# Kernel optimization log

Hardware: AMD Instinct MI355X
Metric: run time of the kernel (lower is better)

## Reference

```python
import jax, jax.numpy as jnp
import numpy as np

B, S, H, NH = 2, 2048, 1024, 16
DK = H // NH


def setup_inputs() -> dict:
    key = jax.random.key(0)
    ks = jax.random.split(key, 11)
    sc = 1.0 / np.sqrt(H)
    return {
        "q": jax.random.normal(ks[0], (B, S, H), jnp.float32),
        "v": jax.random.normal(ks[1], (B, S, H), jnp.float32),
        "k": jax.random.normal(ks[2], (B, S, H), jnp.float32),
        "Wq": jax.random.normal(ks[3], (H, H), jnp.float32) * sc,
        "bq": jax.random.normal(ks[4], (H,), jnp.float32) * 0.01,
        "Wk": jax.random.normal(ks[5], (H, H), jnp.float32) * sc,
        "bk": jax.random.normal(ks[6], (H,), jnp.float32) * 0.01,
        "Wv": jax.random.normal(ks[7], (H, H), jnp.float32) * sc,
        "bv": jax.random.normal(ks[8], (H,), jnp.float32) * 0.01,
        "Wo": jax.random.normal(ks[9], (H, H), jnp.float32) * sc,
        "bo": jax.random.normal(ks[10], (H,), jnp.float32) * 0.01,
    }


def reference(q, v, k, Wq, bq, Wk, bk, Wv, bv, Wo, bo):
    b, s, h = q.shape
    # projections; torch Linear computes x @ W.T + b
    qh = (q @ Wq.T + bq).reshape(b, s, NH, DK).transpose(0, 2, 1, 3)  # [B,NH,S,DK]
    kh = (k @ Wk.T + bk).reshape(b, s, NH, DK).transpose(0, 2, 1, 3)
    vh = (v @ Wv.T + bv).reshape(b, s, NH, DK).transpose(0, 2, 1, 3)
    scores = jnp.einsum("bhqd,bhkd->bhqk", qh, kh) / jnp.sqrt(
        jnp.asarray(DK, qh.dtype))  # [B,NH,S,S]
    probs = jax.nn.softmax(scores, axis=-1)
    ctx = jnp.einsum("bhqk,bhkd->bhqd", probs, vh)  # [B,NH,S,DK]
    concat = ctx.transpose(0, 2, 1, 3).reshape(b, s, h)
    return concat @ Wo.T + bo
```

## Files before the change

### kernel.cpp

```cpp
#include <hip/hip_runtime.h>
#include <cstddef>
#include <cstdint>

typedef _Float16 f16x8 __attribute__((ext_vector_type(8)));
typedef _Float16 f16x4 __attribute__((ext_vector_type(4)));
typedef __fp16   h16x2 __attribute__((ext_vector_type(2)));
typedef float    f32x4 __attribute__((ext_vector_type(4)));

constexpr int B_  = 2;
constexpr int S_  = 2048;
constexpr int H_  = 1024;
constexpr int NH_ = 16;
constexpr int DK_ = 64;
constexpr int M_  = B_ * S_;
constexpr int K_  = H_;

constexpr float SOFF = 4.0f;

#define MFMA32(a, b, c) __builtin_amdgcn_mfma_f32_16x16x32_f16((a), (b), (c), 0, 0, 0)
#define MFMA16(a, b, c) __builtin_amdgcn_mfma_f32_16x16x16f16((a), (b), (c), 0, 0, 0)

__device__ __forceinline__ void glds16(const void* g, void* l) {
    __builtin_amdgcn_global_load_lds(
        (const __attribute__((address_space(1))) void*)g,
        (__attribute__((address_space(3))) void*)l, 16, 0, 0);
}

__device__ __forceinline__ void pk2(f16x4& dst, int half, float a, float b) {
    const h16x2 r = __builtin_amdgcn_cvt_pkrtz(a, b);
    reinterpret_cast<h16x2*>(&dst)[half] = r;
}

struct CvtArgs {
    const float* s[7];
    _Float16*    d[7];
    int          n[7];
};

__global__ __launch_bounds__(256) void cvt7(CvtArgs a)
{
    const int seg = blockIdx.y;
    const int i = (blockIdx.x * 256 + threadIdx.x) * 8;
    if (i + 8 <= a.n[seg]) {
        const float4 v0 = *reinterpret_cast<const float4*>(a.s[seg] + i);
        const float4 v1 = *reinterpret_cast<const float4*>(a.s[seg] + i + 4);
        f16x8 o;
        o[0] = (_Float16)v0.x; o[1] = (_Float16)v0.y;
        o[2] = (_Float16)v0.z; o[3] = (_Float16)v0.w;
        o[4] = (_Float16)v1.x; o[5] = (_Float16)v1.y;
        o[6] = (_Float16)v1.z; o[7] = (_Float16)v1.w;
        *reinterpret_cast<f16x8*>(a.d[seg] + i) = o;
    }
}

struct QkvArgs {
    const _Float16* A[3];
    const _Float16* W[3];
    const float*    bias[3];
    _Float16* dstQ;
    _Float16* dstK;
    _Float16* dstV;
    float qscale;
};

__global__ __launch_bounds__(256) void gemm_qkv(QkvArgs args)
{
    constexpr int BM = 128, BN = 128, BK = 32;
    __shared__ __align__(16) _Float16 sm[8192];
    auto As = reinterpret_cast<_Float16(*)[BK]>(sm);
    auto Ws = reinterpret_cast<_Float16(*)[BK]>(sm + 4096);
    auto Tr = reinterpret_cast<_Float16(*)[64]>(sm);

    const int z = blockIdx.z;
    const _Float16* __restrict__ A = args.A[z];
    const _Float16* __restrict__ W = args.W[z];
    const float* __restrict__ bias = args.bias[z];

    const int t = threadIdx.x;
    const int w = t >> 6, lane = t & 63, quad = lane >> 4, l16 = lane & 15;
    const int m0 = blockIdx.y * BM;
    const int n0 = blockIdx.x * BN;
    const int wr = (w & 1) * 64, wc = (w >> 1) * 64;
    const int srow = lane >> 2, scol = (lane & 3) * 8;

    f32x4 acc[4][4];
#pragma unroll
    for (int i = 0; i < 4; ++i)
#pragma unroll
        for (int j = 0; j < 4; ++j) acc[i][j] = (f32x4){0.f, 0.f, 0.f, 0.f};

    for (int k0 = 0; k0 < K_; k0 += BK) {
        glds16(&A[(size_t)(m0 + w * 32 + srow) * K_ + k0 + scol], &As[w * 32][0]);
        glds16(&A[(size_t)(m0 + w * 32 + 16 + srow) * K_ + k0 + scol], &As[w * 32 + 16][0]);
        glds16(&W[(size_t)(n0 + w * 32 + srow) * K_ + k0 + scol], &Ws[w * 32][0]);
        glds16(&W[(size_t)(n0 + w * 32 + 16 + srow) * K_ + k0 + scol], &Ws[w * 32 + 16][0]);
        __syncthreads();

        f16x8 af[4], bf[4];
#pragma unroll
        for (int i = 0; i < 4; ++i)
            af[i] = *reinterpret_cast<const f16x8*>(&As[wr + i * 16 + l16][quad * 8]);
#pragma unroll
        for (int j = 0; j < 4; ++j)
            bf[j] = *reinterpret_cast<const f16x8*>(&Ws[wc + j * 16 + l16][quad * 8]);
#pragma unroll
        for (int i = 0; i < 4; ++i)
#pragma unroll
            for (int j = 0; j < 4; ++j)
                acc[i][j] = MFMA32(af[i], bf[j], acc[i][j]);
        __syncthreads();
    }

    const float scale = (z == 0) ? args.qscale : 1.0f;
    float bv[4];
#pragma unroll
    for (int j = 0; j < 4; ++j) bv[j] = bias[n0 + wc + j * 16 + l16];

    if (z == 2) {
#pragma unroll
        for (int i = 0; i < 4; ++i) {
            const int sb = m0 + wr + i * 16 + quad * 4;
            const int b = sb >> 11, s = sb & (S_ - 1);
#pragma unroll
            for (int j = 0; j < 4; ++j) {
                const int d = wc + j * 16 + l16;
                const int h = blockIdx.x * 2 + (d >> 6);
                const int dd = d & 63;
                const int kt = s >> 4, dt = dd >> 4;
                f16x4 ov;
#pragma unroll
                for (int r = 0; r < 4; ++r) ov[r] = (_Float16)(acc[i][j][r] + bv[j]);
                _Float16* base = args.dstV +
                    ((((size_t)b * NH_ + h) * 128 + kt) * 4 + dt) * 256;
                *reinterpret_cast<f16x4*>(&base[lane * 4]) = ov;
            }
        }
        return;
    }

    _Float16* dst = (z == 0) ? args.dstQ : args.dstK;
    const int b = m0 >> 11, s0 = m0 & (S_ - 1);
#pragma unroll
    for (int ch = 0; ch < 2; ++ch) {
        __syncthreads();
        if ((w >> 1) == ch) {
#pragma unroll
            for (int i = 0; i < 4; ++i)
#pragma unroll
                for (int j = 0; j < 4; ++j)
#pragma unroll
                    for (int r = 0; r < 4; ++r)
                        Tr[wr + i * 16 + quad * 4 + r][j * 16 + l16] =
                            (_Float16)((acc[i][j][r] + bv[j]) * scale);
        }
        __syncthreads();
        const int h = blockIdx.x * 2 + ch;
        _Float16* dbase = dst + ((size_t)(b * NH_ + h) * S_ + s0) * DK_;
#pragma unroll
        for (int p = 0; p < 4; ++p) {
            const int c = t + p * 256;
            *reinterpret_cast<f16x8*>(&dbase[c * 8]) =
                *reinterpret_cast<const f16x8*>(&Tr[c >> 3][(c & 7) * 8]);
        }
    }
}

__global__ __launch_bounds__(256) void gemm_out(
    const _Float16* __restrict__ A, const _Float16* __restrict__ W,
    const float* __restrict__ bias, float* __restrict__ out)
{
    constexpr int BM = 128, BN = 128, BK = 32;
    __shared__ _Float16 As[BM][BK];
    __shared__ _Float16 Ws[BN][BK];

    const int t = threadIdx.x;
    const int w = t >> 6, lane = t & 63, quad = lane >> 4, l16 = lane & 15;
    const int m0 = blockIdx.y * BM;
    const int n0 = blockIdx.x * BN;
    const int wr = (w & 1) * 64, wc = (w >> 1) * 64;
    const int srow = lane >> 2, scol = (lane & 3) * 8;

    f32x4 acc[4][4];
#pragma unroll
    for (int i = 0; i < 4; ++i)
#pragma unroll
        for (int j = 0; j < 4; ++j) acc[i][j] = (f32x4){0.f, 0.f, 0.f, 0.f};

    for (int k0 = 0; k0 < K_; k0 += BK) {
        glds16(&A[(size_t)(m0 + w * 32 + srow) * K_ + k0 + scol], &As[w * 32][0]);
        glds16(&A[(size_t)(m0 + w * 32 + 16 + srow) * K_ + k0 + scol], &As[w * 32 + 16][0]);
        glds16(&W[(size_t)(n0 + w * 32 + srow) * K_ + k0 + scol], &Ws[w * 32][0]);
        glds16(&W[(size_t)(n0 + w * 32 + 16 + srow) * K_ + k0 + scol], &Ws[w * 32 + 16][0]);
        __syncthreads();

        f16x8 af[4], bf[4];
#pragma unroll
        for (int i = 0; i < 4; ++i)
            af[i] = *reinterpret_cast<const f16x8*>(&As[wr + i * 16 + l16][quad * 8]);
#pragma unroll
        for (int j = 0; j < 4; ++j)
            bf[j] = *reinterpret_cast<const f16x8*>(&Ws[wc + j * 16 + l16][quad * 8]);
#pragma unroll
        for (int i = 0; i < 4; ++i)
#pragma unroll
            for (int j = 0; j < 4; ++j)
                acc[i][j] = MFMA32(af[i], bf[j], acc[i][j]);
        __syncthreads();
    }

    float bv[4];
#pragma unroll
    for (int j = 0; j < 4; ++j) bv[j] = bias[n0 + wc + j * 16 + l16];

#pragma unroll
    for (int i = 0; i < 4; ++i)
#pragma unroll
        for (int j = 0; j < 4; ++j)
#pragma unroll
            for (int r = 0; r < 4; ++r)
                out[(size_t)(m0 + wr + i * 16 + quad * 4 + r) * H_ +
                    n0 + wc + j * 16 + l16] = acc[i][j][r] + bv[j];
}

__global__ __launch_bounds__(256) void attn_mfma(
    const _Float16* __restrict__ qh, const _Float16* __restrict__ kh,
    const _Float16* __restrict__ vfrag, _Float16* __restrict__ ctx)
{
    __shared__ float Ob[4][64][36];
    __shared__ float Ls[4][64];
    __shared__ float Linv[64];

    const int t = threadIdx.x;
    const int w = t >> 6, lane = t & 63, quad = lane >> 4, l16 = lane & 15;
    const int q0 = blockIdx.x * 64;
    const int bh = blockIdx.y;

    const _Float16* qb = qh + (size_t)bh * S_ * DK_;
    const _Float16* kb = kh + (size_t)bh * S_ * DK_;
    const _Float16* vb = vfrag + (size_t)bh * 128 * 4 * 256;

    f16x8 qf[4][2];
#pragma unroll
    for (int qt = 0; qt < 4; ++qt)
#pragma unroll
        for (int h2 = 0; h2 < 2; ++h2)
            qf[qt][h2] = *reinterpret_cast<const f16x8*>(
                &qb[(size_t)(q0 + qt * 16 + l16) * DK_ + h2 * 32 + quad * 8]);

    f32x4 o[4][4];
#pragma unroll
    for (int dt = 0; dt < 4; ++dt)
#pragma unroll
        for (int qt = 0; qt < 4; ++qt) o[dt][qt] = (f32x4){0.f, 0.f, 0.f, 0.f};
    float lp_[4];
#pragma unroll
    for (int qt = 0; qt < 4; ++qt) lp_[qt] = 0.f;

    const _Float16* kptr = kb + (size_t)(w * 16 + l16) * DK_ + quad * 8;
    const _Float16* vptr = vb + (size_t)w * 4 * 256 + lane * 4;

    f16x8 kf0 = *reinterpret_cast<const f16x8*>(kptr);
    f16x8 kf1 = *reinterpret_cast<const f16x8*>(kptr + 32);

    for (int ti = 0; ti < 32; ++ti) {
        f16x4 vf[4];
#pragma unroll
        for (int dt = 0; dt < 4; ++dt)
            vf[dt] = *reinterpret_cast<const f16x4*>(vptr + dt * 256);
        vptr += 4 * 4 * 256;

        const _Float16* nkp = (ti < 31) ? kptr + 64 * DK_ : kptr;
        const f16x8 nk0 = *reinterpret_cast<const f16x8*>(nkp);
        const f16x8 nk1 = *reinterpret_cast<const f16x8*>(nkp + 32);
        kptr = nkp;

        f32x4 sc[4];
#pragma unroll
        for (int qt = 0; qt < 4; ++qt) {
            sc[qt] = (f32x4){-SOFF, -SOFF, -SOFF, -SOFF};
            sc[qt] = MFMA32(kf0, qf[qt][0], sc[qt]);
            sc[qt] = MFMA32(kf1, qf[qt][1], sc[qt]);
        }

        f16x4 pf[4];
#pragma unroll
        for (int qt = 0; qt < 4; ++qt) {
            const float p0 = __builtin_amdgcn_exp2f(sc[qt][0]);
            const float p1 = __builtin_amdgcn_exp2f(sc[qt][1]);
            const float p2 = __builtin_amdgcn_exp2f(sc[qt][2]);
            const float p3 = __builtin_amdgcn_exp2f(sc[qt][3]);
            lp_[qt] += (p0 + p1) + (p2 + p3);
            f16x4 pv;
            pk2(pv, 0, p0, p1);
            pk2(pv, 1, p2, p3);
            pf[qt] = pv;
        }

#pragma unroll
        for (int dt = 0; dt < 4; ++dt)
#pragma unroll
            for (int qt = 0; qt < 4; ++qt)
                o[dt][qt] = MFMA16(vf[dt], pf[qt], o[dt][qt]);

        kf0 = nk0;
        kf1 = nk1;
    }

#pragma unroll
    for (int qt = 0; qt < 4; ++qt) {
        float l = lp_[qt];
        l += __shfl_xor(l, 16);
        l += __shfl_xor(l, 32);
        if (quad == 0) Ls[w][qt * 16 + l16] = l;
    }
    __syncthreads();
    if (t < 64)
        Linv[t] = 1.f / (((Ls[0][t] + Ls[1][t]) + (Ls[2][t] + Ls[3][t])));

    const int b = bh >> 4, hh = bh & 15;
    const int dg = t & 3, qq = t >> 2;
#pragma unroll
    for (int ph = 0; ph < 2; ++ph) {
        __syncthreads();
#pragma unroll
        for (int dl = 0; dl < 2; ++dl) {
            const int dt = ph * 2 + dl;
#pragma unroll
            for (int qt = 0; qt < 4; ++qt)
                *reinterpret_cast<f32x4*>(
                    &Ob[w][qt * 16 + l16][dl * 16 + quad * 4]) = o[dt][qt];
        }
        __syncthreads();
        f32x4 s0 = (f32x4){0.f, 0.f, 0.f, 0.f};
        f32x4 s1 = (f32x4){0.f, 0.f, 0.f, 0.f};
#pragma unroll
        for (int ww = 0; ww < 4; ++ww) {
            s0 += *reinterpret_cast<const f32x4*>(&Ob[ww][qq][dg * 8]);
            s1 += *reinterpret_cast<const f32x4*>(&Ob[ww][qq][dg * 8 + 4]);
        }
        const float li = Linv[qq];
        f16x8 ov;
#pragma unroll
        for (int r = 0; r < 4; ++r) {
            ov[r]     = (_Float16)(s0[r] * li);
            ov[4 + r] = (_Float16)(s1[r] * li);
        }
        *reinterpret_cast<f16x8*>(
            &ctx[((size_t)b * S_ + q0 + qq) * H_ + hh * 64 + ph * 32 + dg * 8]) = ov;
    }
}

extern "C" void kernel_launch(void* const* d_in, const int* in_sizes, int n_in,
                              void* d_out, int out_size, void* d_ws,
                              size_t ws_size, hipStream_t stream)
{
    (void)in_sizes; (void)n_in; (void)out_size; (void)ws_size;
    const float* q  = (const float*)d_in[0];
    const float* v  = (const float*)d_in[1];
    const float* k  = (const float*)d_in[2];
    const float* Wq = (const float*)d_in[3];
    const float* bq = (const float*)d_in[4];
    const float* Wk = (const float*)d_in[5];
    const float* bk = (const float*)d_in[6];
    const float* Wv = (const float*)d_in[7];
    const float* bv = (const float*)d_in[8];
    const float* Wo = (const float*)d_in[9];
    const float* bo = (const float*)d_in[10];
    float* out = (float*)d_out;

    constexpr size_t NACT = (size_t)M_ * K_;
    constexpr size_t NW   = (size_t)H_ * H_;
    _Float16* p = (_Float16*)d_ws;
    _Float16* q16  = p;
    _Float16* k16  = p + NACT;
    _Float16* v16  = p + 2 * NACT;
    _Float16* w16q = p + 3 * NACT;
    _Float16* w16k = w16q + NW;
    _Float16* w16v = w16k + NW;
    _Float16* w16o = w16v + NW;
    _Float16* qhd  = w16o + NW;
    _Float16* khd  = qhd + NACT;
    _Float16* vfr  = khd + NACT;
    _Float16* ctx  = q16;

    CvtArgs ca;
    ca.s[0] = q;  ca.d[0] = q16;  ca.n[0] = (int)NACT;
    ca.s[1] = v;  ca.d[1] = v16;  ca.n[1] = (int)NACT;
    ca.s[2] = k;  ca.d[2] = k16;  ca.n[2] = (int)NACT;
    ca.s[3] = Wq; ca.d[3] = w16q; ca.n[3] = (int)NW;
    ca.s[4] = Wk; ca.d[4] = w16k; ca.n[4] = (int)NW;
    ca.s[5] = Wv; ca.d[5] = w16v; ca.n[5] = (int)NW;
    ca.s[6] = Wo; ca.d[6] = w16o; ca.n[6] = (int)NW;
    cvt7<<<dim3(2048, 7), 256, 0, stream>>>(ca);

    QkvArgs ga;
    ga.A[0] = q16;  ga.W[0] = w16q; ga.bias[0] = bq;
    ga.A[1] = k16;  ga.W[1] = w16k; ga.bias[1] = bk;
    ga.A[2] = v16;  ga.W[2] = w16v; ga.bias[2] = bv;
    ga.dstQ = qhd;  ga.dstK = khd;  ga.dstV = vfr;
    ga.qscale = 0.125f * 1.4426950408889634f;

    gemm_qkv<<<dim3(H_ / 128, M_ / 128, 3), 256, 0, stream>>>(ga);

    attn_mfma<<<dim3(S_ / 64, B_ * NH_), 256, 0, stream>>>(qhd, khd, vfr, ctx);

    gemm_out<<<dim3(H_ / 128, M_ / 128), 256, 0, stream>>>(ctx, w16o, bo, out);
}
```

Baseline: 236.6 us.

## Pipeline QK scores one step ahead, use 32-wide PV MFMA, remap grids

The attention loop now handles two 64-key tiles per iteration. It computes the next pair's QK scores after the PV MFMAs, wrapped in s_setprio, so score MFMAs overlap exp work across iterations. V is stored in a new fragment layout that allows 16x16x32 MFMAs for P·V instead of 16x16x16. The attention grid is flattened and remapped so blocks of the same head land on the same XCD for L2 reuse. The output GEMM tile shrinks to 64x128, doubling block count to improve occupancy at the cost of less reuse per block.

```diff
diff --git a/kernel.cpp b/kernel.cpp
--- a/kernel.cpp
+++ b/kernel.cpp
@@ -6,6 +6,7 @@
 typedef _Float16 f16x4 __attribute__((ext_vector_type(4)));
 typedef __fp16   h16x2 __attribute__((ext_vector_type(2)));
 typedef float    f32x4 __attribute__((ext_vector_type(4)));
+typedef float    f32x2 __attribute__((ext_vector_type(2)));
 
 constexpr int B_  = 2;
 constexpr int S_  = 2048;
@@ -18,17 +19,11 @@
 constexpr float SOFF = 4.0f;
 
 #define MFMA32(a, b, c) __builtin_amdgcn_mfma_f32_16x16x32_f16((a), (b), (c), 0, 0, 0)
-#define MFMA16(a, b, c) __builtin_amdgcn_mfma_f32_16x16x16f16((a), (b), (c), 0, 0, 0)
 
 __device__ __forceinline__ void glds16(const void* g, void* l) {
     __builtin_amdgcn_global_load_lds(
         (const __attribute__((address_space(1))) void*)g,
         (__attribute__((address_space(3))) void*)l, 16, 0, 0);
-}
-
-__device__ __forceinline__ void pk2(f16x4& dst, int half, float a, float b) {
-    const h16x2 r = __builtin_amdgcn_cvt_pkrtz(a, b);
-    reinterpret_cast<h16x2*>(&dst)[half] = r;
 }
 
 struct CvtArgs {
@@ -121,18 +116,20 @@
         for (int i = 0; i < 4; ++i) {
             const int sb = m0 + wr + i * 16 + quad * 4;
             const int b = sb >> 11, s = sb & (S_ - 1);
+            const int kt = s >> 4;
+            const int w4 = kt & 3, tIdx = kt >> 2;
+            const int p16 = tIdx >> 1, sub = tIdx & 1;
 #pragma unroll
             for (int j = 0; j < 4; ++j) {
                 const int d = wc + j * 16 + l16;
                 const int h = blockIdx.x * 2 + (d >> 6);
-                const int dd = d & 63;
-                const int kt = s >> 4, dt = dd >> 4;
+                const int dt = (d & 63) >> 4;
                 f16x4 ov;
 #pragma unroll
                 for (int r = 0; r < 4; ++r) ov[r] = (_Float16)(acc[i][j][r] + bv[j]);
-                _Float16* base = args.dstV +
-                    ((((size_t)b * NH_ + h) * 128 + kt) * 4 + dt) * 256;
-                *reinterpret_cast<f16x4*>(&base[lane * 4]) = ov;
+                _Float16* base = args.dstV + ((size_t)b * NH_ + h) * 131072
+                    + (size_t)(((w4 * 16 + p16) * 4 + dt) * 512 + lane * 8 + sub * 4);
+                *reinterpret_cast<f16x4*>(base) = ov;
             }
         }
         return;
@@ -169,7 +166,7 @@
     const _Float16* __restrict__ A, const _Float16* __restrict__ W,
     const float* __restrict__ bias, float* __restrict__ out)
 {
-    constexpr int BM = 128, BN = 128, BK = 32;
+    constexpr int BM = 64, BN = 128, BK = 32;
     __shared__ _Float16 As[BM][BK];
     __shared__ _Float16 Ws[BN][BK];
 
@@ -177,49 +174,48 @@
     const int w = t >> 6, lane = t & 63, quad = lane >> 4, l16 = lane & 15;
     const int m0 = blockIdx.y * BM;
     const int n0 = blockIdx.x * BN;
-    const int wr = (w & 1) * 64, wc = (w >> 1) * 64;
+    const int wc = w * 32;
     const int srow = lane >> 2, scol = (lane & 3) * 8;
 
-    f32x4 acc[4][4];
+    f32x4 acc[4][2];
 #pragma unroll
     for (int i = 0; i < 4; ++i)
 #pragma unroll
-        for (int j = 0; j < 4; ++j) acc[i][j] = (f32x4){0.f, 0.f, 0.f, 0.f};
+        for (int j = 0; j < 2; ++j) acc[i][j] = (f32x4){0.f, 0.f, 0.f, 0.f};
 
     for (int k0 = 0; k0 < K_; k0 += BK) {
-        glds16(&A[(size_t)(m0 + w * 32 + srow) * K_ + k0 + scol], &As[w * 32][0]);
-        glds16(&A[(size_t)(m0 + w * 32 + 16 + srow) * K_ + k0 + scol], &As[w * 32 + 16][0]);
+        glds16(&A[(size_t)(m0 + w * 16 + srow) * K_ + k0 + scol], &As[w * 16][0]);
         glds16(&W[(size_t)(n0 + w * 32 + srow) * K_ + k0 + scol], &Ws[w * 32][0]);
         glds16(&W[(size_t)(n0 + w * 32 + 16 + srow) * K_ + k0 + scol], &Ws[w * 32 + 16][0]);
         __syncthreads();
 
-        f16x8 af[4], bf[4];
+        f16x8 af[4], bf[2];
 #pragma unroll
         for (int i = 0; i < 4; ++i)
-            af[i] = *reinterpret_cast<const f16x8*>(&As[wr + i * 16 + l16][quad * 8]);
-#pragma unroll
-        for (int j = 0; j < 4; ++j)
+            af[i] = *reinterpret_cast<const f16x8*>(&As[i * 16 + l16][quad * 8]);
+#pragma unroll
+        for (int j = 0; j < 2; ++j)
             bf[j] = *reinterpret_cast<const f16x8*>(&Ws[wc + j * 16 + l16][quad * 8]);
 #pragma unroll
         for (int i = 0; i < 4; ++i)
 #pragma unroll
-            for (int j = 0; j < 4; ++j)
+            for (int j = 0; j < 2; ++j)
                 acc[i][j] = MFMA32(af[i], bf[j], acc[i][j]);
         __syncthreads();
     }
 
-    float bv[4];
-#pragma unroll
-    for (int j = 0; j < 4; ++j) bv[j] = bias[n0 + wc + j * 16 + l16];
+    float bvv[2];
+#pragma unroll
+    for (int j = 0; j < 2; ++j) bvv[j] = bias[n0 + wc + j * 16 + l16];
 
 #pragma unroll
     for (int i = 0; i < 4; ++i)
 #pragma unroll
-        for (int j = 0; j < 4; ++j)
+        for (int j = 0; j < 2; ++j)
 #pragma unroll
             for (int r = 0; r < 4; ++r)
-                out[(size_t)(m0 + wr + i * 16 + quad * 4 + r) * H_ +
-                    n0 + wc + j * 16 + l16] = acc[i][j][r] + bv[j];
+                out[(size_t)(m0 + i * 16 + quad * 4 + r) * H_ +
+                    n0 + wc + j * 16 + l16] = acc[i][j][r] + bvv[j];
 }
 
 __global__ __launch_bounds__(256) void attn_mfma(
@@ -232,12 +228,15 @@
 
     const int t = threadIdx.x;
     const int w = t >> 6, lane = t & 63, quad = lane >> 4, l16 = lane & 15;
-    const int q0 = blockIdx.x * 64;
-    const int bh = blockIdx.y;
+
+    const int lin = blockIdx.x;
+    const int xcd = lin & 7, slot = lin >> 3;
+    const int bh = xcd + 8 * (slot >> 5);
+    const int q0 = (slot & 31) * 64;
 
     const _Float16* qb = qh + (size_t)bh * S_ * DK_;
     const _Float16* kb = kh + (size_t)bh * S_ * DK_;
-    const _Float16* vb = vfrag + (size_t)bh * 128 * 4 * 256;
+    const _Float16* vb = vfrag + (size_t)bh * 131072;
 
     f16x8 qf[4][2];
 #pragma unroll
@@ -247,68 +246,89 @@
             qf[qt][h2] = *reinterpret_cast<const f16x8*>(
                 &qb[(size_t)(q0 + qt * 16 + l16) * DK_ + h2 * 32 + quad * 8]);
 
+    const f32x4 msoff = (f32x4){-SOFF, -SOFF, -SOFF, -SOFF};
+
     f32x4 o[4][4];
 #pragma unroll
     for (int dt = 0; dt < 4; ++dt)
 #pragma unroll
         for (int qt = 0; qt < 4; ++qt) o[dt][qt] = (f32x4){0.f, 0.f, 0.f, 0.f};
-    float lp_[4];
-#pragma unroll
-    for (int qt = 0; qt < 4; ++qt) lp_[qt] = 0.f;
-
-    const _Float16* kptr = kb + (size_t)(w * 16 + l16) * DK_ + quad * 8;
-    const _Float16* vptr = vb + (size_t)w * 4 * 256 + lane * 4;
-
-    f16x8 kf0 = *reinterpret_cast<const f16x8*>(kptr);
-    f16x8 kf1 = *reinterpret_cast<const f16x8*>(kptr + 32);
-
-    for (int ti = 0; ti < 32; ++ti) {
-        f16x4 vf[4];
+    f32x2 lp2[4];
+#pragma unroll
+    for (int qt = 0; qt < 4; ++qt) lp2[qt] = (f32x2){0.f, 0.f};
+
+    const _Float16* kp = kb + (size_t)(w * 16 + l16) * DK_ + quad * 8;
+    const _Float16* vp = vb + (size_t)w * 32768 + lane * 8;
+
+    f32x4 scA[4], scB[4];
+    {
+        const f16x8 kA0 = *reinterpret_cast<const f16x8*>(kp);
+        const f16x8 kA1 = *reinterpret_cast<const f16x8*>(kp + 32);
+        const f16x8 kB0 = *reinterpret_cast<const f16x8*>(kp + 64 * DK_);
+        const f16x8 kB1 = *reinterpret_cast<const f16x8*>(kp + 64 * DK_ + 32);
+        kp += 128 * DK_;
+#pragma unroll
+        for (int qt = 0; qt < 4; ++qt) {
+            f32x4 t0 = MFMA32(kA0, qf[qt][0], msoff);
+            scA[qt] = MFMA32(kA1, qf[qt][1], t0);
+            f32x4 t1 = MFMA32(kB0, qf[qt][0], msoff);
+            scB[qt] = MFMA32(kB1, qf[qt][1], t1);
+        }
+    }
+
+    for (int p = 0; p < 16; ++p) {
+        const _Float16* nk = (p < 15) ? kp : (kp - 128 * DK_);
+        const f16x8 nA0 = *reinterpret_cast<const f16x8*>(nk);
+        const f16x8 nA1 = *reinterpret_cast<const f16x8*>(nk + 32);
+        const f16x8 nB0 = *reinterpret_cast<const f16x8*>(nk + 64 * DK_);
+        const f16x8 nB1 = *reinterpret_cast<const f16x8*>(nk + 64 * DK_ + 32);
+        kp = nk + 128 * DK_;
+
+        f16x8 vf8[4];
 #pragma unroll
         for (int dt = 0; dt < 4; ++dt)
-            vf[dt] = *reinterpret_cast<const f16x4*>(vptr + dt * 256);
-        vptr += 4 * 4 * 256;
-
-        const _Float16* nkp = (ti < 31) ? kptr + 64 * DK_ : kptr;
-        const f16x8 nk0 = *reinterpret_cast<const f16x8*>(nkp);
-        const f16x8 nk1 = *reinterpret_cast<const f16x8*>(nkp + 32);
-        kptr = nkp;
-
-        f32x4 sc[4];
+            vf8[dt] = *reinterpret_cast<const f16x8*>(vp + dt * 512);
+        vp += 2048;
+
+        f16x8 pf8[4];
 #pragma unroll
         for (int qt = 0; qt < 4; ++qt) {
-            sc[qt] = (f32x4){-SOFF, -SOFF, -SOFF, -SOFF};
-            sc[qt] = MFMA32(kf0, qf[qt][0], sc[qt]);
-            sc[qt] = MFMA32(kf1, qf[qt][1], sc[qt]);
-        }
-
-        f16x4 pf[4];
+            const float a0 = __builtin_amdgcn_exp2f(scA[qt][0]);
+            const float a1 = __builtin_amdgcn_exp2f(scA[qt][1]);
+            const float a2 = __builtin_amdgcn_exp2f(scA[qt][2]);
+            const float a3 = __builtin_amdgcn_exp2f(scA[qt][3]);
+            const float b0 = __builtin_amdgcn_exp2f(scB[qt][0]);
+            const float b1 = __builtin_amdgcn_exp2f(scB[qt][1]);
+            const float b2 = __builtin_amdgcn_exp2f(scB[qt][2]);
+            const float b3 = __builtin_amdgcn_exp2f(scB[qt][3]);
+            lp2[qt] += ((f32x2){a0, a1} + (f32x2){a2, a3}) +
+                       ((f32x2){b0, b1} + (f32x2){b2, b3});
+            h16x2* ph = reinterpret_cast<h16x2*>(&pf8[qt]);
+            ph[0] = __builtin_amdgcn_cvt_pkrtz(a0, a1);
+            ph[1] = __builtin_amdgcn_cvt_pkrtz(a2, a3);
+            ph[2] = __builtin_amdgcn_cvt_pkrtz(b0, b1);
+            ph[3] = __builtin_amdgcn_cvt_pkrtz(b2, b3);
+        }
+
+        __builtin_amdgcn_s_setprio(1);
+#pragma unroll
+        for (int dt = 0; dt < 4; ++dt)
+#pragma unroll
+            for (int qt = 0; qt < 4; ++qt)
+                o[dt][qt] = MFMA32(vf8[dt], pf8[qt], o[dt][qt]);
 #pragma unroll
         for (int qt = 0; qt < 4; ++qt) {
-            const float p0 = __builtin_amdgcn_exp2f(sc[qt][0]);
-            const float p1 = __builtin_amdgcn_exp2f(sc[qt][1]);
-            const float p2 = __builtin_amdgcn_exp2f(sc[qt][2]);
-            const float p3 = __builtin_amdgcn_exp2f(sc[qt][3]);
-            lp_[qt] += (p0 + p1) + (p2 + p3);
-            f16x4 pv;
-            pk2(pv, 0, p0, p1);
-            pk2(pv, 1, p2, p3);
-            pf[qt] = pv;
-        }
-
-#pragma unroll
-        for (int dt = 0; dt < 4; ++dt)
-#pragma unroll
-            for (int qt = 0; qt < 4; ++qt)
-                o[dt][qt] = MFMA16(vf[dt], pf[qt], o[dt][qt]);
-
-        kf0 = nk0;
-        kf1 = nk1;
+            f32x4 t0 = MFMA32(nA0, qf[qt][0], msoff);
+            scA[qt] = MFMA32(nA1, qf[qt][1], t0);
+            f32x4 t1 = MFMA32(nB0, qf[qt][0], msoff);
+            scB[qt] = MFMA32(nB1, qf[qt][1], t1);
+        }
+        __builtin_amdgcn_s_setprio(0);
     }
 
 #pragma unroll
     for (int qt = 0; qt < 4; ++qt) {
-        float l = lp_[qt];
+        float l = lp2[qt][0] + lp2[qt][1];
         l += __shfl_xor(l, 16);
         l += __shfl_xor(l, 32);
         if (quad == 0) Ls[w][qt * 16 + l16] = l;
@@ -402,7 +422,7 @@
 
     gemm_qkv<<<dim3(H_ / 128, M_ / 128, 3), 256, 0, stream>>>(ga);
 
-    attn_mfma<<<dim3(S_ / 64, B_ * NH_), 256, 0, stream>>>(qhd, khd, vfr, ctx);
-
-    gemm_out<<<dim3(H_ / 128, M_ / 128), 256, 0, stream>>>(ctx, w16o, bo, out);
-}
+    attn_mfma<<<dim3(S_ / 64 * B_ * NH_), 256, 0, stream>>>(qhd, khd, vfr, ctx);
+
+    gemm_out<<<dim3(H_ / 128, M_ / 64), 256, 0, stream>>>(ctx, w16o, bo, out);
+}
```

After: 225.9 us. -4.5%, faster.
